# Optimization experiments

Hardware: AMD Instinct MI355X
Metric: run time of the kernel (lower is better)

## Reference

```python
import jax, jax.numpy as jnp
import numpy as np
import math

T = 4096          # num tokens (== context_window_len)
IN_SIZE = 2048    # model dim
HEAD_SIZE = 128   # per-head dim


def setup_inputs() -> dict:
    key = jax.random.key(0)
    kx, kq, kk, kv = jax.random.split(key, 4)
    scale = 1.0 / math.sqrt(IN_SIZE)
    x = jax.random.normal(kx, (T, IN_SIZE), dtype=jnp.float32)
    # eqx.nn.Linear(in, out) weight has shape [out, in], applied as W @ x
    Wq = jax.random.normal(kq, (HEAD_SIZE, IN_SIZE), dtype=jnp.float32) * scale
    Wk = jax.random.normal(kk, (HEAD_SIZE, IN_SIZE), dtype=jnp.float32) * scale
    Wv = jax.random.normal(kv, (HEAD_SIZE, IN_SIZE), dtype=jnp.float32) * scale
    return {"x": x, "Wq": Wq, "Wk": Wk, "Wv": Wv}


def reference(x, Wq, Wk, Wv):
    # q, k, v: [T, head_size]
    q = x @ Wq.T
    k = x @ Wk.T
    v = x @ Wv.T
    # scores: [T, T]
    scores = (q @ k.T) / math.sqrt(HEAD_SIZE)
    num_toks = x.shape[0]
    # causal mask: True above the diagonal (masked out)
    causal_mask = ~jnp.tril(jnp.ones((num_toks, num_toks), dtype=bool))
    masked = jnp.where(causal_mask, -jnp.inf, scores)
    attn = jax.nn.softmax(masked, axis=-1)
    return attn @ v
```

## Files before the change

kernel.cpp:

```cpp
#include <hip/hip_runtime.h>
#include <hip/hip_bf16.h>

#define T_TOK 4096
#define D_IN  2048
#define HS    128
#define CKV   4
#define NCH   16

typedef unsigned short u16;
typedef __attribute__((ext_vector_type(8))) __bf16 bf16x8;
typedef __attribute__((ext_vector_type(4))) float f32x4;
typedef __attribute__((ext_vector_type(4))) unsigned short us4;
typedef __attribute__((ext_vector_type(8))) unsigned short us8;

#define GLOBAL_AS __attribute__((address_space(1)))
#define LDS_AS    __attribute__((address_space(3)))

__device__ __forceinline__ void async_ld16(const void* g, void* l) {
  __builtin_amdgcn_global_load_lds((GLOBAL_AS void*)(void*)g, (LDS_AS void*)l, 16, 0, 0);
}

__device__ __forceinline__ u16 f2bf(float v) {
  return __builtin_bit_cast(u16, __float2bfloat16(v));
}

__device__ __forceinline__ bool detect_f32(const u16* in, int tid, int* sflag) {
  if (tid < 64) {
    int cnt = 0;
#pragma unroll
    for (int j = 0; j < 8; j++) {
      u16 v = in[(tid * 8 + j) * 2];
      cnt += (((v >> 7) & 0xFF) >= 0xBF) ? 1 : 0;
    }
#pragma unroll
    for (int off = 1; off < 64; off <<= 1) cnt += __shfl_xor(cnt, off);
    if (tid == 0) *sflag = (cnt > 8) ? 1 : 0;
  }
  __syncthreads();
  return (*sflag != 0);
}

__global__ __launch_bounds__(256) void conv3_kernel(
    const u16* __restrict__ w0, const u16* __restrict__ w1,
    const u16* __restrict__ w2, u16* __restrict__ o0,
    u16* __restrict__ o1, u16* __restrict__ o2, int* __restrict__ flag) {
  __shared__ int sflag;
  const int mat = blockIdx.x >> 7;
  const int blk = blockIdx.x & 127;
  const u16* in = (mat == 0) ? w0 : ((mat == 1) ? w1 : w2);
  u16* out = (mat == 0) ? o0 : ((mat == 1) ? o1 : o2);
  const int tid = threadIdx.x;
  const bool isf32 = detect_f32(in, tid, &sflag);
  if (tid == 0 && mat == 0 && blk == 0) *flag = isf32 ? 1 : 0;
  const size_t base = ((size_t)blk * 256 + tid) * 8;
  if (isf32) {
    const float* f = (const float*)in;
    us4 a, b;
#pragma unroll
    for (int j = 0; j < 4; j++) a[j] = f2bf(f[base + j]);
#pragma unroll
    for (int j = 0; j < 4; j++) b[j] = f2bf(f[base + 4 + j]);
    *(us4*)(out + base) = a;
    *(us4*)(out + base + 4) = b;
  } else {
    *(us8*)(out + base) = *(const us8*)(in + base);
  }
}

__global__ __launch_bounds__(256, 2) void qkv_kernel(
    const u16* __restrict__ x, const u16* __restrict__ Wq,
    const u16* __restrict__ Wk, const u16* __restrict__ Wv,
    u16* __restrict__ Q, u16* __restrict__ K, u16* __restrict__ Vt)
{
  __shared__ __align__(16) u16 As[2][64 * 64];
  __shared__ __align__(16) u16 Bs[2][128 * 64];
  __shared__ int sflag;

  const int mat = blockIdx.y;
  const u16* W = (mat == 0) ? Wq : ((mat == 1) ? Wk : Wv);
  const int mtile = blockIdx.x;
  const int tid = threadIdx.x;
  const int wv = tid >> 6, lane = tid & 63, l15 = lane & 15, quad = lane >> 4;
  const int row0 = mtile * 64;

  const bool isf32 = detect_f32(x, tid, &sflag);

  f32x4 acc[8];
#pragma unroll
  for (int i = 0; i < 8; i++) acc[i] = (f32x4)0.0f;

  const int s0 = tid * 2;
  const int ar = s0 >> 3;
  const int ac0 = (s0 & 7) ^ (ar & 7);
  const int ac1 = ((s0 + 1) & 7) ^ (ar & 7);

  f32x4 pa[4];
  auto loadA_f32 = [&](int k0) {
    const float* xf = (const float*)x + (size_t)(row0 + ar) * D_IN + k0;
    pa[0] = *(const f32x4*)(xf + ac0 * 8);
    pa[1] = *(const f32x4*)(xf + ac0 * 8 + 4);
    pa[2] = *(const f32x4*)(xf + ac1 * 8);
    pa[3] = *(const f32x4*)(xf + ac1 * 8 + 4);
  };
  auto writeA_f32 = [&](int buf) {
    us8 c0, c1;
#pragma unroll
    for (int j = 0; j < 4; j++) {
      c0[j] = f2bf(pa[0][j]); c0[4 + j] = f2bf(pa[1][j]);
      c1[j] = f2bf(pa[2][j]); c1[4 + j] = f2bf(pa[3][j]);
    }
    *(us8*)((char*)As[buf] + (size_t)s0 * 16) = c0;
    *(us8*)((char*)As[buf] + (size_t)(s0 + 1) * 16) = c1;
  };
  auto stageA_bf16 = [&](int k0, int buf) {
#pragma unroll
    for (int j = 0; j < 2; j++) {
      int s = (wv * 2 + j) * 64 + lane;
      int r = s >> 3, cs = s & 7, c = cs ^ (r & 7);
      async_ld16(x + (size_t)(row0 + r) * D_IN + k0 + c * 8,
                 (char*)As[buf] + (size_t)(wv * 2 + j) * 1024);
    }
  };
  auto stageB = [&](int k0, int buf) {
#pragma unroll
    for (int j = 0; j < 4; j++) {
      int s = (wv * 4 + j) * 64 + lane;
      int n = s >> 3, cs = s & 7, c = cs ^ (n & 7);
      async_ld16(W + (size_t)n * D_IN + k0 + c * 8,
                 (char*)Bs[buf] + (size_t)(wv * 4 + j) * 1024);
    }
  };

  stageB(0, 0);
  if (isf32) loadA_f32(0); else stageA_bf16(0, 0);

  for (int kt = 0; kt < 32; kt++) {
    const int cur = kt & 1;
    if (isf32) writeA_f32(cur);
    __syncthreads();
    if (kt < 31) {
      stageB((kt + 1) * 64, 1 - cur);
      if (isf32) loadA_f32((kt + 1) * 64); else stageA_bf16((kt + 1) * 64, 1 - cur);
    }
#pragma unroll
    for (int kc = 0; kc < 2; kc++) {
      const int rA = 16 * wv + l15;
      const int cl = kc * 4 + quad;
      bf16x8 a = *(const bf16x8*)((const char*)As[cur] + (rA * 8 + (cl ^ (rA & 7))) * 16);
#pragma unroll
      for (int nt = 0; nt < 8; nt++) {
        int n = 16 * nt + l15;
        bf16x8 b = *(const bf16x8*)((const char*)Bs[cur] + (n * 8 + (cl ^ (n & 7))) * 16);
        acc[nt] = __builtin_amdgcn_mfma_f32_16x16x32_bf16(a, b, acc[nt], 0, 0, 0);
      }
    }
  }

  if (mat < 2) {
    u16* out = (mat == 0) ? Q : K;
#pragma unroll
    for (int nt = 0; nt < 8; nt++)
#pragma unroll
      for (int r = 0; r < 4; r++) {
        int m = row0 + 16 * wv + quad * 4 + r;
        int n = 16 * nt + l15;
        out[(size_t)m * HS + n] = f2bf(acc[nt][r]);
      }
  } else {
#pragma unroll
    for (int nt = 0; nt < 8; nt++) {
      int n = 16 * nt + l15;
      int mb = row0 + 16 * wv + quad * 4;
      us4 pk;
#pragma unroll
      for (int r = 0; r < 4; r++) pk[r] = f2bf(acc[nt][r]);
      *(us4*)(Vt + (size_t)n * T_TOK + mb) = pk;
    }
  }
}

__global__ __launch_bounds__(256, 2) void attn_split_kernel(
    const u16* __restrict__ Q, const u16* __restrict__ Kg,
    const u16* __restrict__ Vt, float* __restrict__ Opart,
    float* __restrict__ mstat, float* __restrict__ lstat)
{
  __shared__ __align__(16) u16 Ks[2][64 * 128];
  __shared__ __align__(16) u16 Vs[2][128 * 64];
  __shared__ __align__(16) u16 Ps[4 * 16 * 64];

  const int qtile = 63 - (int)blockIdx.x;
  const int ch = blockIdx.y;
  if (4 * ch > qtile) return;
  const int t0 = 4 * ch;
  const int nsteps = min(CKV, qtile + 1 - t0);
  const int q0 = qtile * 64;
  const int slot = 64 * ch - 2 * ch * (ch - 1) + (qtile - 4 * ch);

  const int tid = threadIdx.x;
  const int wv = tid >> 6, lane = tid & 63, l15 = lane & 15, quad = lane >> 4;

  bf16x8 qf[4];
#pragma unroll
  for (int kc = 0; kc < 4; kc++)
    qf[kc] = *(const bf16x8*)(Q + (size_t)(q0 + 16 * wv + l15) * HS + kc * 32 + quad * 8);

  f32x4 o[8];
#pragma unroll
  for (int i = 0; i < 8; i++) o[i] = (f32x4)0.0f;
  float mrun[4], lrun[4];
#pragma unroll
  for (int r = 0; r < 4; r++) { mrun[r] = -1e30f; lrun[r] = 0.0f; }

  const float sc = 0.12752761571239668f;

  auto stage = [&](int t, int buf) {
#pragma unroll
    for (int j = 0; j < 4; j++) {
      int s = (wv * 4 + j) * 64 + lane;
      int n = s >> 4, cs = s & 15, c = cs ^ (n & 7);
      async_ld16(Kg + (size_t)(t * 64 + n) * HS + c * 8,
                 (char*)Ks[buf] + (size_t)(wv * 4 + j) * 1024);
    }
#pragma unroll
    for (int j = 0; j < 4; j++) {
      int s = (wv * 4 + j) * 64 + lane;
      int vr = s >> 3, cs = s & 7, c = cs ^ (vr & 7);
      async_ld16(Vt + (size_t)vr * T_TOK + t * 64 + c * 8,
                 (char*)Vs[buf] + (size_t)(wv * 4 + j) * 1024);
    }
  };

  stage(t0, 0);
  for (int i = 0; i < nsteps; i++) {
    const int cur = i & 1;
    const int t = t0 + i;
    __syncthreads();
    if (i + 1 < nsteps) stage(t + 1, 1 - cur);

    f32x4 sacc[4];
#pragma unroll
    for (int nt = 0; nt < 4; nt++) sacc[nt] = (f32x4)0.0f;
#pragma unroll
    for (int kc = 0; kc < 4; kc++) {
      const int cl = kc * 4 + quad;
#pragma unroll
      for (int nt = 0; nt < 4; nt++) {
        int n = 16 * nt + l15;
        bf16x8 b = *(const bf16x8*)((const char*)Ks[cur] + (n * 16 + (cl ^ (n & 7))) * 16);
        sacc[nt] = __builtin_amdgcn_mfma_f32_16x16x32_bf16(qf[kc], b, sacc[nt], 0, 0, 0);
      }
    }

    float s2[4][4];
    const bool diag = (t == qtile);
#pragma unroll
    for (int nt = 0; nt < 4; nt++)
#pragma unroll
      for (int r = 0; r < 4; r++) {
        float v = sacc[nt][r] * sc;
        if (diag) {
          int qr = q0 + 16 * wv + quad * 4 + r;
          int kr = t * 64 + 16 * nt + l15;
          if (kr > qr) v = -1e30f;
        }
        s2[nt][r] = v;
      }

    float mnew[4], alpha[4];
#pragma unroll
    for (int r = 0; r < 4; r++) {
      float tmax = fmaxf(fmaxf(s2[0][r], s2[1][r]), fmaxf(s2[2][r], s2[3][r]));
#pragma unroll
      for (int off = 1; off < 16; off <<= 1) tmax = fmaxf(tmax, __shfl_xor(tmax, off));
      mnew[r] = fmaxf(mrun[r], tmax);
      alpha[r] = exp2f(mrun[r] - mnew[r]);
      mrun[r] = mnew[r];
    }
    float p[4][4];
#pragma unroll
    for (int r = 0; r < 4; r++) {
      float s = 0.0f;
#pragma unroll
      for (int nt = 0; nt < 4; nt++) { p[nt][r] = exp2f(s2[nt][r] - mnew[r]); s += p[nt][r]; }
#pragma unroll
      for (int off = 1; off < 16; off <<= 1) s += __shfl_xor(s, off);
      lrun[r] = lrun[r] * alpha[r] + s;
    }
#pragma unroll
    for (int c = 0; c < 8; c++)
#pragma unroll
      for (int r = 0; r < 4; r++) o[c][r] *= alpha[r];

    u16* Pw = Ps + wv * 1024;
#pragma unroll
    for (int nt = 0; nt < 4; nt++)
#pragma unroll
      for (int r = 0; r < 4; r++) {
        int row = quad * 4 + r;
        int col = nt * 16 + l15;
        int cc = col >> 3, wi = col & 7;
        Pw[(row * 8 + (cc ^ (row & 7))) * 8 + wi] = f2bf(p[nt][r]);
      }

#pragma unroll
    for (int kc = 0; kc < 2; kc++) {
      const int cl = kc * 4 + quad;
      bf16x8 a = *(const bf16x8*)((const char*)Pw + (l15 * 8 + (cl ^ (l15 & 7))) * 16);
#pragma unroll
      for (int c = 0; c < 8; c++) {
        int vr = 16 * c + l15;
        bf16x8 b = *(const bf16x8*)((const char*)Vs[cur] + (vr * 8 + (cl ^ (vr & 7))) * 16);
        o[c] = __builtin_amdgcn_mfma_f32_16x16x32_bf16(a, b, o[c], 0, 0, 0);
      }
    }
  }

  float* po = Opart + (size_t)slot * 64 * 128;
#pragma unroll
  for (int c = 0; c < 8; c++)
#pragma unroll
    for (int r = 0; r < 4; r++) {
      int ml = 16 * wv + quad * 4 + r;
      po[ml * 128 + 16 * c + l15] = o[c][r];
    }
  if (l15 == 0) {
#pragma unroll
    for (int r = 0; r < 4; r++) {
      int ml = 16 * wv + quad * 4 + r;
      mstat[slot * 64 + ml] = mrun[r];
      lstat[slot * 64 + ml] = lrun[r];
    }
  }
}

__global__ __launch_bounds__(256) void combine_kernel(
    const float* __restrict__ Opart, const float* __restrict__ mstat,
    const float* __restrict__ lstat, void* __restrict__ out_v,
    const int* __restrict__ dflag)
{
  const int q = blockIdx.x;
  const int cb = blockIdx.y;
  const int tid = threadIdx.x;
  const int row = tid >> 2;
  const int col = cb * 32 + (tid & 3) * 8;
  const int nch = (q + 4) / 4;
  const bool of32 = (*dflag != 0);

  float M = -1e30f;
  {
    int base = 0;
    for (int c = 0; c < nch; c++) {
      int s = base + q - 4 * c;
      M = fmaxf(M, mstat[s * 64 + row]);
      base += 64 - 4 * c;
    }
  }
  float l = 0.0f;
  float acc[8];
#pragma unroll
  for (int j = 0; j < 8; j++) acc[j] = 0.0f;
  {
    int base = 0;
    for (int c = 0; c < nch; c++) {
      int s = base + q - 4 * c;
      float w = exp2f(mstat[s * 64 + row] - M);
      l += w * lstat[s * 64 + row];
      const float* op = Opart + ((size_t)s * 64 + row) * 128 + col;
      f32x4 a = *(const f32x4*)op;
      f32x4 b = *(const f32x4*)(op + 4);
#pragma unroll
      for (int j = 0; j < 4; j++) { acc[j] += w * a[j]; acc[4 + j] += w * b[j]; }
      base += 64 - 4 * c;
    }
  }
  const float inv = 1.0f / l;
  const size_t goff = (size_t)(q * 64 + row) * HS + col;
  if (of32) {
    float* out = (float*)out_v + goff;
    f32x4 r0, r1;
#pragma unroll
    for (int j = 0; j < 4; j++) { r0[j] = acc[j] * inv; r1[j] = acc[4 + j] * inv; }
    *(f32x4*)out = r0;
    *(f32x4*)(out + 4) = r1;
  } else {
    u16* out = (u16*)out_v + goff;
    us4 r0, r1;
#pragma unroll
    for (int j = 0; j < 4; j++) { r0[j] = f2bf(acc[j] * inv); r1[j] = f2bf(acc[4 + j] * inv); }
    *(us4*)out = r0;
    *(us4*)(out + 4) = r1;
  }
}

extern "C" void kernel_launch(void* const* d_in, const int* in_sizes, int n_in,
                              void* d_out, int out_size, void* d_ws, size_t ws_size,
                              hipStream_t stream) {
  const u16* x  = (const u16*)d_in[0];
  const u16* Wq = (const u16*)d_in[1];
  const u16* Wk = (const u16*)d_in[2];
  const u16* Wv = (const u16*)d_in[3];

  float* Opart = (float*)d_ws;
  float* mstat = Opart + (size_t)544 * 64 * 128;
  float* lstat = mstat + (size_t)544 * 64;

  u16* Wqb = (u16*)(lstat + (size_t)544 * 64);
  u16* Wkb = Wqb + (size_t)HS * D_IN;
  u16* Wvb = Wkb + (size_t)HS * D_IN;
  u16* Q   = Wvb + (size_t)HS * D_IN;
  u16* K   = Q   + (size_t)T_TOK * HS;
  u16* Vt  = K   + (size_t)T_TOK * HS;
  int* flag = (int*)(Vt + (size_t)T_TOK * HS);

  conv3_kernel<<<384, 256, 0, stream>>>(Wq, Wk, Wv, Wqb, Wkb, Wvb, flag);
  qkv_kernel<<<dim3(64, 3), 256, 0, stream>>>(x, Wqb, Wkb, Wvb, Q, K, Vt);
  attn_split_kernel<<<dim3(64, NCH), 256, 0, stream>>>(Q, K, Vt, Opart, mstat, lstat);
  combine_kernel<<<dim3(64, 4), 256, 0, stream>>>(Opart, mstat, lstat, d_out, flag);
}
```

Baseline: 147.6 us.

## Split-K the QKV projection across four slices with a separate reduction kernel

```diff
diff --git a/kernel.cpp b/kernel.cpp
--- a/kernel.cpp
+++ b/kernel.cpp
@@ -70,7 +70,7 @@
 __global__ __launch_bounds__(256, 2) void qkv_kernel(
     const u16* __restrict__ x, const u16* __restrict__ Wq,
     const u16* __restrict__ Wk, const u16* __restrict__ Wv,
-    u16* __restrict__ Q, u16* __restrict__ K, u16* __restrict__ Vt)
+    float* __restrict__ Ppart)
 {
   __shared__ __align__(16) u16 As[2][64 * 64];
   __shared__ __align__(16) u16 Bs[2][128 * 64];
@@ -79,6 +79,8 @@
   const int mat = blockIdx.y;
   const u16* W = (mat == 0) ? Wq : ((mat == 1) ? Wk : Wv);
   const int mtile = blockIdx.x;
+  const int ks = blockIdx.z;
+  const int kbase = ks * 512;
   const int tid = threadIdx.x;
   const int wv = tid >> 6, lane = tid & 63, l15 = lane & 15, quad = lane >> 4;
   const int row0 = mtile * 64;
@@ -131,16 +133,17 @@
     }
   };
 
-  stageB(0, 0);
-  if (isf32) loadA_f32(0); else stageA_bf16(0, 0);
-
-  for (int kt = 0; kt < 32; kt++) {
+  stageB(kbase, 0);
+  if (isf32) loadA_f32(kbase); else stageA_bf16(kbase, 0);
+
+  for (int kt = 0; kt < 8; kt++) {
     const int cur = kt & 1;
     if (isf32) writeA_f32(cur);
     __syncthreads();
-    if (kt < 31) {
-      stageB((kt + 1) * 64, 1 - cur);
-      if (isf32) loadA_f32((kt + 1) * 64); else stageA_bf16((kt + 1) * 64, 1 - cur);
+    if (kt < 7) {
+      stageB(kbase + (kt + 1) * 64, 1 - cur);
+      if (isf32) loadA_f32(kbase + (kt + 1) * 64);
+      else stageA_bf16(kbase + (kt + 1) * 64, 1 - cur);
     }
 #pragma unroll
     for (int kc = 0; kc < 2; kc++) {
@@ -156,25 +159,50 @@
     }
   }
 
+  float* po = Ppart + (((size_t)ks * 3 + mat) * 64 + mtile) * 8192;
   if (mat < 2) {
-    u16* out = (mat == 0) ? Q : K;
 #pragma unroll
     for (int nt = 0; nt < 8; nt++)
 #pragma unroll
       for (int r = 0; r < 4; r++) {
-        int m = row0 + 16 * wv + quad * 4 + r;
+        int m = 16 * wv + quad * 4 + r;
         int n = 16 * nt + l15;
-        out[(size_t)m * HS + n] = f2bf(acc[nt][r]);
+        po[m * 128 + n] = acc[nt][r];
       }
   } else {
 #pragma unroll
     for (int nt = 0; nt < 8; nt++) {
       int n = 16 * nt + l15;
-      int mb = row0 + 16 * wv + quad * 4;
-      us4 pk;
-#pragma unroll
-      for (int r = 0; r < 4; r++) pk[r] = f2bf(acc[nt][r]);
-      *(us4*)(Vt + (size_t)n * T_TOK + mb) = pk;
+      int mb = 16 * wv + quad * 4;
+      f32x4 pk;
+#pragma unroll
+      for (int r = 0; r < 4; r++) pk[r] = acc[nt][r];
+      *(f32x4*)(po + (size_t)n * 64 + mb) = pk;
+    }
+  }
+}
+
+__global__ __launch_bounds__(256) void qkv_reduce_kernel(
+    const float* __restrict__ Ppart, u16* __restrict__ Q,
+    u16* __restrict__ K, u16* __restrict__ Vt)
+{
+  const int mtile = blockIdx.x;
+  const int mat = blockIdx.y;
+  const int tid = threadIdx.x;
+  const size_t ksS = (size_t)3 * 64 * 8192;
+  const float* base = Ppart + ((size_t)mat * 64 + mtile) * 8192;
+
+#pragma unroll
+  for (int e = 0; e < 32; e++) {
+    int j = e * 256 + tid;
+    float s = base[j] + base[j + ksS] + base[j + 2 * ksS] + base[j + 3 * ksS];
+    if (mat < 2) {
+      int m = j >> 7, n = j & 127;
+      u16* out = (mat == 0) ? Q : K;
+      out[(size_t)(mtile * 64 + m) * HS + n] = f2bf(s);
+    } else {
+      int n = j >> 6, m = j & 63;
+      Vt[(size_t)n * T_TOK + mtile * 64 + m] = f2bf(s);
     }
   }
 }
@@ -412,8 +440,11 @@
   u16* Vt  = K   + (size_t)T_TOK * HS;
   int* flag = (int*)(Vt + (size_t)T_TOK * HS);
 
+  float* qkvP = (float*)((char*)d_ws + ((size_t)32 << 20));
+
   conv3_kernel<<<384, 256, 0, stream>>>(Wq, Wk, Wv, Wqb, Wkb, Wvb, flag);
-  qkv_kernel<<<dim3(64, 3), 256, 0, stream>>>(x, Wqb, Wkb, Wvb, Q, K, Vt);
+  qkv_kernel<<<dim3(64, 3, 4), 256, 0, stream>>>(x, Wqb, Wkb, Wvb, qkvP);
+  qkv_reduce_kernel<<<dim3(64, 3), 256, 0, stream>>>(qkvP, Q, K, Vt);
   attn_split_kernel<<<dim3(64, NCH), 256, 0, stream>>>(Q, K, Vt, Opart, mstat, lstat);
   combine_kernel<<<dim3(64, 4), 256, 0, stream>>>(Opart, mstat, lstat, d_out, flag);
 }
```

After: 142.7 us. 3.3% less time.
